# Optimization experiments

Hardware: AMD Instinct MI355X
Metric: run time of the kernel (lower is better)

Reference implementation:

```python
import jax, jax.numpy as jnp
from jax import lax
import numpy as np

D_MODEL = 384; D_INNER = 768; D_STATE = 16; D_CONV = 4; DT_RANK = 24
BATCH = 2; SEQ = 4096


def _mamba(x, in_w, conv_w, conv_b, xproj_w, dt_w, dt_b, A_log, Dp, out_w):
    # x: [B, L, D_MODEL]
    xz = x @ in_w.T                                   # [B, L, 2*D_INNER]
    xi, z = jnp.split(xz, 2, axis=-1)
    xc = jnp.swapaxes(xi, 1, 2)                       # [B, D_INNER, L]
    xc = lax.conv_general_dilated(xc, conv_w, (1,), [(D_CONV - 1, 0)],
                                  feature_group_count=D_INNER)  # causal depthwise conv
    xc = jax.nn.silu(xc + conv_b[None, :, None])
    xc = jnp.swapaxes(xc, 1, 2)                       # [B, L, D_INNER]
    xdbl = xc @ xproj_w.T                             # [B, L, DT_RANK + 2*D_STATE]
    dt = xdbl[..., :DT_RANK]
    Bm = xdbl[..., DT_RANK:DT_RANK + D_STATE]
    Cm = xdbl[..., DT_RANK + D_STATE:]
    delta = jax.nn.softplus(dt @ dt_w.T + dt_b)       # [B, L, D_INNER]
    A = -jnp.exp(A_log)                               # [D_INNER, D_STATE]

    def step(h, inp):
        d_t, x_t, B_t, C_t = inp                      # [B,Di],[B,Di],[B,N],[B,N]
        dA = jnp.exp(d_t[..., None] * A)              # [B, Di, N]
        h = dA * h + (d_t * x_t)[..., None] * B_t[:, None, :]
        return h, jnp.einsum('bdn,bn->bd', h, C_t)

    xs = tuple(jnp.swapaxes(a, 0, 1) for a in (delta, xc, Bm, Cm))  # time-major
    h0 = jnp.zeros((x.shape[0], D_INNER, D_STATE), x.dtype)
    _, ys = lax.scan(step, h0, xs)                    # ys: [L, B, D_INNER]
    y = jnp.swapaxes(ys, 0, 1) + xc * Dp              # skip term D*x
    return (y * jax.nn.silu(z)) @ out_w.T             # [B, L, D_MODEL]


def _forward(x, fp, bp, c_w, c_b, gn_w, gn_b):
    xt = jnp.swapaxes(x, 1, 2)                        # [B, L, C]
    yf = _mamba(xt, *fp)
    yb = _mamba(xt[:, ::-1, :], *bp)                  # note: source does NOT flip back
    y = jnp.concatenate([yf, yb], axis=2)             # [B, L, 2C]
    y = jnp.swapaxes(y, 1, 2)                         # [B, 2C, L]
    y = jnp.einsum('oc,bcl->bol', c_w[:, :, 0], y) + c_b[None, :, None]  # 1x1 conv
    a, b = jnp.split(y, 2, axis=1)                    # GLU over channel dim
    y = a * jax.nn.sigmoid(b)                         # [B, C, L]
    mu = y.mean(axis=(1, 2), keepdims=True)           # GroupNorm(1, C)
    var = y.var(axis=(1, 2), keepdims=True)
    y = (y - mu) / jnp.sqrt(var + 1e-5)
    return y * gn_w[None, :, None] + gn_b[None, :, None]


def setup_inputs() -> dict:
    key = jax.random.key(0)
    it = iter(jax.random.split(key, 20))

    def nrm(shape, s=0.02):
        return jax.random.normal(next(it), shape, jnp.float32) * s

    def mamba_params(pref):
        return {
            pref + 'in_w': nrm((2 * D_INNER, D_MODEL)),
            pref + 'conv_w': nrm((D_INNER, 1, D_CONV), 0.3),
            pref + 'conv_b': nrm((D_INNER,)),
            pref + 'xproj_w': nrm((DT_RANK + 2 * D_STATE, D_INNER)),
            pref + 'dt_w': nrm((D_INNER, DT_RANK), 0.1),
            pref + 'dt_b': nrm((D_INNER,)),
            pref + 'A_log': jnp.log(jnp.tile(jnp.arange(1.0, D_STATE + 1.0, dtype=jnp.float32), (D_INNER, 1))),
            pref + 'D': jnp.ones((D_INNER,), jnp.float32),
            pref + 'out_w': nrm((D_MODEL, D_INNER)),
        }

    inp = {'x': jax.random.normal(next(it), (BATCH, D_MODEL, SEQ), jnp.float32)}
    inp.update(mamba_params('f_'))
    inp.update(mamba_params('b_'))
    inp['c_w'] = nrm((2 * D_MODEL, 2 * D_MODEL, 1))
    inp['c_b'] = nrm((2 * D_MODEL,))
    inp['gn_w'] = jnp.ones((D_MODEL,), jnp.float32)
    inp['gn_b'] = jnp.zeros((D_MODEL,), jnp.float32)
    return inp


def reference(x, f_in_w, f_conv_w, f_conv_b, f_xproj_w, f_dt_w, f_dt_b, f_A_log, f_D, f_out_w,
              b_in_w, b_conv_w, b_conv_b, b_xproj_w, b_dt_w, b_dt_b, b_A_log, b_D, b_out_w,
              c_w, c_b, gn_w, gn_b):
    fp = (f_in_w, f_conv_w, f_conv_b, f_xproj_w, f_dt_w, f_dt_b, f_A_log, f_D, f_out_w)
    bp = (b_in_w, b_conv_w, b_conv_b, b_xproj_w, b_dt_w, b_dt_b, b_A_log, b_D, b_out_w)
    return _forward(x, fp, bp, c_w, c_b, gn_w, gn_b)
```

## Files before the change

### kernel.cpp

```cpp
#include <hip/hip_runtime.h>
#include <hip/hip_bf16.h>
#include <hip/hip_fp16.h>

typedef unsigned short u16;
typedef unsigned int   u32;
typedef __bf16  bf16x8 __attribute__((ext_vector_type(8)));
typedef float   f32x4  __attribute__((ext_vector_type(4)));

#define BL   8192
#define LSEQ 4096
#define DI   768
#define CHUNK 32
#define NCHUNK (LSEQ / CHUNK)
#define CTC  16
#define LOG2E 1.44269504088896340736f

#define LOAD_LDS16(g, l) __builtin_amdgcn_global_load_lds( \
    (const __attribute__((address_space(1))) void*)(g), \
    (__attribute__((address_space(3))) void*)(l), 16, 0, 0)

static __device__ __forceinline__ float bf2f(u16 u) {
    union { float f; u32 i; } v; v.i = ((u32)u) << 16; return v.f;
}
static __device__ __forceinline__ u16 f2bs(float f) {
    union { float f; u32 i; } v; v.f = f;
    u32 r = v.i + 0x7fffu + ((v.i >> 16) & 1u);
    return (u16)(r >> 16);
}
static __device__ __forceinline__ float ldf(const void* p, size_t i, int f32) {
    return f32 ? ((const float*)p)[i] : bf2f(((const u16*)p)[i]);
}

__global__ void detect_dtype(const void* __restrict__ gnw, int* __restrict__ flag) {
    u32 bits = *(const u32*)gnw;
    *flag = ((bits & 0xFFFFu) == 0u) ? 1 : 0;
}

__global__ void check_apow(const void* __restrict__ a_f, const void* __restrict__ a_b,
                           int* __restrict__ apow, const int* __restrict__ flag) {
    int f = *flag;
    __shared__ int ok;
    if (threadIdx.x == 0) ok = 1;
    __syncthreads();
    for (int i = threadIdx.x; i < 2 * 12288; i += 256) {
        const void* a = (i >= 12288) ? a_b : a_f;
        int idx = i % 12288;
        int d = idx >> 4, n = idx & 15;
        float An = __expf(ldf(a, idx, f));
        float rf = __expf(ldf(a, d * 16, f)) * (float)(n + 1);
        if (fabsf(An - rf) > 1e-5f * fabsf(rf)) ok = 0;
    }
    __syncthreads();
    if (threadIdx.x == 0) *apow = ok;
}

__global__ void cvt_bf16_3(const void* __restrict__ s0, const void* __restrict__ s1,
                           const void* __restrict__ s2, u16* __restrict__ dst,
                           int n0, int n1, int ntot, const int* __restrict__ flag) {
    int i = blockIdx.x * 256 + threadIdx.x;
    if (i >= ntot) return;
    int f = *flag;
    const void* s; size_t off;
    if (i < n0)      { s = s0; off = i; }
    else if (i < n1) { s = s1; off = i - n0; }
    else             { s = s2; off = i - n1; }
    dst[i] = f ? f2bs(((const float*)s)[off]) : ((const u16*)s)[off];
}

__global__ void cvt_conv(const void* __restrict__ cw_f, const void* __restrict__ cw_b,
                         const void* __restrict__ cb_f, const void* __restrict__ cb_b,
                         float* __restrict__ cwf, float* __restrict__ cbf,
                         const int* __restrict__ flag) {
    int i = blockIdx.x * 256 + threadIdx.x;
    int f = *flag;
    if (i < 2 * 3072)
        cwf[i] = ldf(i < 3072 ? cw_f : cw_b, i % 3072, f);
    int j = i - 2 * 3072;
    if (j >= 0 && j < 2 * 768)
        cbf[j] = ldf(j < 768 ? cb_f : cb_b, j % 768, f);
}

__global__ void transpose_x(const void* __restrict__ x, u16* __restrict__ xT,
                            const int* __restrict__ flag) {
    __shared__ u16 tile[32][33];
    int f = *flag;
    int b  = blockIdx.z;
    int l0 = blockIdx.x * 32, c0 = blockIdx.y * 32;
    int li = threadIdx.x, ci = threadIdx.y;
    for (int cc = ci; cc < 32; cc += 8) {
        size_t idx = (size_t)(b * 384 + c0 + cc) * LSEQ + l0 + li;
        tile[cc][li] = f ? f2bs(((const float*)x)[idx]) : ((const u16*)x)[idx];
    }
    __syncthreads();
    for (int lc = ci; lc < 32; lc += 8)
        xT[(size_t)(b * LSEQ + l0 + lc) * 384 + c0 + li] = tile[li][lc];
}

__global__ void build_wcomb(const void* __restrict__ xp_f, const void* __restrict__ dtw_f,
                            const void* __restrict__ xp_b, const void* __restrict__ dtw_b,
                            u16* __restrict__ Wc, const int* __restrict__ flag) {
    int f = *flag;
    int dir = blockIdx.y;
    const void* xp  = dir ? xp_b  : xp_f;
    const void* dtw = dir ? dtw_b : dtw_f;
    u16* W = Wc + (size_t)dir * 896 * 768;
    int idx = blockIdx.x * 256 + threadIdx.x;
    if (idx >= 896 * 768) return;
    int nrow = idx / 768, k = idx - nrow * 768;
    float v = 0.f;
    if (nrow < 768) {
#pragma unroll
        for (int r = 0; r < 24; r++)
            v = fmaf(ldf(dtw, nrow * 24 + r, f), ldf(xp, r * 768 + k, f), v);
    } else if (nrow < 800) {
        v = ldf(xp, (24 + (nrow - 768)) * 768 + k, f);
    }
    W[idx] = f2bs(v);
}

__global__ __launch_bounds__(256) void gemm_mfma(
    const u16* __restrict__ A, int lda, size_t aStr,
    const u16* __restrict__ W, int ldw, size_t wStr,
    int K, int NB, int Nstore, int mode,
    u16* __restrict__ ob0, u16* __restrict__ ob1,
    float* __restrict__ of0, float* __restrict__ of1,
    const void* __restrict__ bias0, const void* __restrict__ bias1,
    const int* __restrict__ flag) {
    __shared__ __align__(16) u16 lA[128 * 32];
    __shared__ __align__(16) u16 lB[128 * 32];
    const int f = *flag;
    const int tid = threadIdx.x;
    const int wave = tid >> 6, lane = tid & 63;
    const int flat = blockIdx.x;
    const int mb = flat & 63;
    const int rest = flat >> 6;
    const int nb = rest % NB;
    const int dir = rest / NB;
    const int m0 = mb * 128, n0 = nb * 128;
    const int wr = (wave >> 1) * 64, wc = (wave & 1) * 64;
    const int fr = lane & 15, fq = lane >> 4;
    const void* bias = dir ? bias1 : bias0;

    f32x4 acc[4][4];
#pragma unroll
    for (int i = 0; i < 4; i++)
#pragma unroll
        for (int j = 0; j < 4; j++) acc[i][j] = 0.f;

    const int srow = wave * 16 + (lane >> 2);
    const int scol = (lane & 3) * 8;
    const u16* gA0 = A + (size_t)dir * aStr + (size_t)(m0 + srow) * lda + scol;
    const u16* gA1 = gA0 + (size_t)64 * lda;
    const u16* gB0 = W + (size_t)dir * wStr + (size_t)(n0 + srow) * ldw + scol;
    const u16* gB1 = gB0 + (size_t)64 * ldw;
    u16* dA0 = &lA[wave * 512];
    u16* dA1 = &lA[2048 + wave * 512];
    u16* dB0 = &lB[wave * 512];
    u16* dB1 = &lB[2048 + wave * 512];

    for (int k0 = 0; k0 < K; k0 += 32) {
        __syncthreads();
        LOAD_LDS16(gA0, dA0);
        LOAD_LDS16(gA1, dA1);
        LOAD_LDS16(gB0, dB0);
        LOAD_LDS16(gB1, dB1);
        gA0 += 32; gA1 += 32; gB0 += 32; gB1 += 32;
        __syncthreads();
        bf16x8 af[4], bfr[4];
#pragma unroll
        for (int i = 0; i < 4; i++) af[i]  = *(const bf16x8*)&lA[(wr + i * 16 + fr) * 32 + fq * 8];
#pragma unroll
        for (int j = 0; j < 4; j++) bfr[j] = *(const bf16x8*)&lB[(wc + j * 16 + fr) * 32 + fq * 8];
#pragma unroll
        for (int i = 0; i < 4; i++)
#pragma unroll
            for (int j = 0; j < 4; j++)
                acc[i][j] = __builtin_amdgcn_mfma_f32_16x16x32_bf16(af[i], bfr[j], acc[i][j], 0, 0, 0);
    }

    const int lr = (lane >> 4) * 4, lc = lane & 15;
#pragma unroll
    for (int i = 0; i < 4; i++) {
#pragma unroll
        for (int j = 0; j < 4; j++) {
#pragma unroll
            for (int rg = 0; rg < 4; rg++) {
                int m = m0 + wr + i * 16 + lr + rg;
                int n = n0 + wc + j * 16 + lc;
                if (n >= Nstore) continue;
                float v = acc[i][j][rg];
                if (mode == 0) {
                    int bI = m >> 12, l = m & 4095;
                    size_t r = dir ? ((size_t)bI * LSEQ + (LSEQ - 1 - l)) : (size_t)m;
                    if (n < 768) ob0[(size_t)dir * BL * DI + r * 768 + n] = f2bs(v);
                    else         ob1[(size_t)dir * BL * DI + r * 768 + (n - 768)] = f2bs(v);
                } else if (mode == 1) {
                    if (n < 768) {
                        float xp = v + ldf(bias, n, f);
                        float sp = fmaxf(xp, 0.f) + __logf(1.f + __expf(-fabsf(xp)));
                        ((__half*)ob0)[(size_t)dir * BL * DI + (size_t)m * 768 + n] = __float2half_rn(sp);
                    } else {
                        of1[(size_t)dir * BL * 32 + (size_t)m * 32 + (n - 768)] = v;
                    }
                } else if (mode == 2) {
                    ob0[(size_t)m * 768 + dir * 384 + n] = f2bs(v);
                } else {
                    of0[(size_t)m * 768 + n] = v + ldf(bias, n, f);
                }
            }
        }
    }
}

__global__ __launch_bounds__(256) void conv_silu(
    const u16* __restrict__ xi, u16* __restrict__ xc,
    const float* __restrict__ cwf, const float* __restrict__ cbf) {
    int gid = blockIdx.x * 256 + threadIdx.x;
    int dg = gid % 96;
    int rest = gid / 96;
    int tc = rest % (LSEQ / CTC);
    int bd = rest / (LSEQ / CTC);
    int dir = bd >> 1;
    int d0 = dg * 8;
    float w[32], bias[8];
#pragma unroll
    for (int q = 0; q < 8; q++) *(float4*)&w[q * 4] = *(const float4*)&cwf[dir * 3072 + d0 * 4 + q * 4];
    *(float4*)&bias[0] = *(const float4*)&cbf[dir * 768 + d0];
    *(float4*)&bias[4] = *(const float4*)&cbf[dir * 768 + d0 + 4];
    size_t rowbase = (size_t)bd * LSEQ;
    int t0 = tc * CTC;
    uint4 zero; zero.x = zero.y = zero.z = zero.w = 0u;
    uint4 win[4];
#pragma unroll
    for (int i = 0; i < 3; i++) {
        int tt = t0 - 3 + i;
        win[i] = (tt >= 0) ? *(const uint4*)&xi[(rowbase + tt) * DI + d0] : zero;
    }
    uint4 nxt = *(const uint4*)&xi[(rowbase + t0) * DI + d0];
#pragma unroll 4
    for (int i = 0; i < CTC; i++) {
        win[3] = nxt;
        if (i + 1 < CTC) nxt = *(const uint4*)&xi[(rowbase + t0 + i + 1) * DI + d0];
        float acc[8];
#pragma unroll
        for (int c = 0; c < 8; c++) acc[c] = bias[c];
#pragma unroll
        for (int tap = 0; tap < 4; tap++) {
            const u16* pv = (const u16*)&win[tap];
#pragma unroll
            for (int c = 0; c < 8; c++)
                acc[c] = fmaf(w[c * 4 + tap], bf2f(pv[c]), acc[c]);
        }
        u16 ov[8];
#pragma unroll
        for (int c = 0; c < 8; c++) ov[c] = f2bs(acc[c] / (1.f + __expf(-acc[c])));
        *(uint4*)&xc[(rowbase + t0 + i) * DI + d0] = *(const uint4*)ov;
        win[0] = win[1]; win[1] = win[2]; win[2] = win[3];
    }
}

__global__ __launch_bounds__(256) void scan_phase1(
    const __half* __restrict__ delta, const u16* __restrict__ xc,
    const float* __restrict__ bc,
    __half* __restrict__ S, __half* __restrict__ sumdl,
    const void* __restrict__ alog_f, const void* __restrict__ alog_b,
    const int* __restrict__ flag, const int* __restrict__ apow) {
    int f = *flag, ap = *apow;
    int dblk = blockIdx.x, chunk = blockIdx.y, bd = blockIdx.z;
    int dir = bd >> 1;
    const void* alog = dir ? alog_b : alog_f;
    int d = dblk * 256 + threadIdx.x;
    size_t rowbase = (size_t)bd * LSEQ;
    float h[16];
#pragma unroll
    for (int n = 0; n < 16; n++) h[n] = 0.f;
    float An2_0 = -__expf(ldf(alog, d * 16, f)) * LOG2E;
    int t0 = chunk * CHUNK;
    size_t off = (rowbase + t0) * DI + d;
    const float* bcG = bc + (rowbase + t0) * 32;
    float sd = 0.f;
    if (ap) {
#pragma unroll 2
        for (int i = 0; i < CHUNK; i++, off += DI) {
            float Bv[16];
#pragma unroll
            for (int q = 0; q < 4; q++) *(float4*)&Bv[q * 4] = *(const float4*)&bcG[(size_t)i * 32 + q * 4];
            float dl = __half2float(delta[off]);
            float u = dl * bf2f(xc[off]);
            sd += dl;
            float e[16];
            float e1 = exp2f(dl * An2_0);
            e[0]=e1; e[1]=e1*e1; e[2]=e[1]*e1; e[3]=e[1]*e[1];
            e[4]=e[3]*e[0]; e[5]=e[3]*e[1]; e[6]=e[3]*e[2]; e[7]=e[3]*e[3];
            e[8]=e[7]*e[0]; e[9]=e[7]*e[1]; e[10]=e[7]*e[2]; e[11]=e[7]*e[3];
            e[12]=e[7]*e[4]; e[13]=e[7]*e[5]; e[14]=e[7]*e[6]; e[15]=e[7]*e[7];
#pragma unroll
            for (int n = 0; n < 16; n++) h[n] = fmaf(e[n], h[n], u * Bv[n]);
        }
    } else {
        float An2[16];
#pragma unroll
        for (int n = 0; n < 16; n++) An2[n] = -__expf(ldf(alog, d * 16 + n, f)) * LOG2E;
#pragma unroll 2
        for (int i = 0; i < CHUNK; i++, off += DI) {
            float Bv[16];
#pragma unroll
            for (int q = 0; q < 4; q++) *(float4*)&Bv[q * 4] = *(const float4*)&bcG[(size_t)i * 32 + q * 4];
            float dl = __half2float(delta[off]);
            float u = dl * bf2f(xc[off]);
            sd += dl;
#pragma unroll
            for (int n = 0; n < 16; n++)
                h[n] = fmaf(exp2f(dl * An2[n]), h[n], u * Bv[n]);
        }
    }
    __half hs[16];
#pragma unroll
    for (int n = 0; n < 16; n++) hs[n] = __float2half(h[n]);
    __half* Sp = S + (((size_t)bd * NCHUNK + chunk) * 768 + d) * 16;
    *(uint4*)&Sp[0] = *(const uint4*)&hs[0];
    *(uint4*)&Sp[8] = *(const uint4*)&hs[8];
    sumdl[((size_t)bd * NCHUNK + chunk) * 768 + d] = __float2half(sd);
}

__global__ __launch_bounds__(256) void scan_fixup(
    __half* __restrict__ S, const __half* __restrict__ sumdl,
    const void* __restrict__ alog_f, const void* __restrict__ alog_b,
    const int* __restrict__ flag) {
    int f = *flag;
    int gid = blockIdx.x * 256 + threadIdx.x;
    int bd = gid / 12288;
    int r  = gid % 12288;
    int d = r >> 4, n = r & 15;
    const void* alog = (bd >> 1) ? alog_b : alog_f;
    float An2 = -__expf(ldf(alog, d * 16 + n, f)) * LOG2E;
    float h = 0.f;
#pragma unroll 4
    for (int c = 0; c < NCHUNK; c++) {
        size_t sidx = (((size_t)bd * NCHUNK + c) * 768 + d) * 16 + n;
        float s  = __half2float(S[sidx]);
        float sd = __half2float(sumdl[((size_t)bd * NCHUNK + c) * 768 + d]);
        S[sidx] = __float2half(h);
        h = fmaf(exp2f(An2 * sd), h, s);
    }
}

__global__ __launch_bounds__(256) void scan_phase3(
    const __half* __restrict__ delta, const u16* __restrict__ xc,
    const float* __restrict__ bc, const u16* __restrict__ zz,
    const __half* __restrict__ S, u16* __restrict__ yg,
    const void* __restrict__ alog_f, const void* __restrict__ alog_b,
    const void* __restrict__ D_f, const void* __restrict__ D_b,
    const int* __restrict__ flag, const int* __restrict__ apow) {
    int f = *flag, ap = *apow;
    int dblk = blockIdx.x, chunk = blockIdx.y, bd = blockIdx.z;
    int dir = bd >> 1;
    const void* alog = dir ? alog_b : alog_f;
    const void* Dp   = dir ? D_b   : D_f;
    int d = dblk * 256 + threadIdx.x;
    size_t rowbase = (size_t)bd * LSEQ;
    float An2_0 = -__expf(ldf(alog, d * 16, f)) * LOG2E;
    float h[16];
    {
        const __half* Sp = S + (((size_t)bd * NCHUNK + chunk) * 768 + d) * 16;
        uint4 sv0 = *(const uint4*)&Sp[0];
        uint4 sv1 = *(const uint4*)&Sp[8];
        const __half* ph0 = (const __half*)&sv0;
        const __half* ph1 = (const __half*)&sv1;
#pragma unroll
        for (int n = 0; n < 8; n++) { h[n] = __half2float(ph0[n]); h[n + 8] = __half2float(ph1[n]); }
    }
    float Dd = ldf(Dp, d, f);
    int t0 = chunk * CHUNK;
    size_t off = (rowbase + t0) * DI + d;
    const float* bcG = bc + (rowbase + t0) * 32;
    if (ap) {
#pragma unroll 2
        for (int i = 0; i < CHUNK; i++, off += DI) {
            float Bv[16], Cv[16];
#pragma unroll
            for (int q = 0; q < 4; q++) *(float4*)&Bv[q * 4] = *(const float4*)&bcG[(size_t)i * 32 + q * 4];
#pragma unroll
            for (int q = 0; q < 4; q++) *(float4*)&Cv[q * 4] = *(const float4*)&bcG[(size_t)i * 32 + 16 + q * 4];
            float dl = __half2float(delta[off]);
            float xf = bf2f(xc[off]);
            float u = dl * xf;
            float e[16];
            float e1 = exp2f(dl * An2_0);
            e[0]=e1; e[1]=e1*e1; e[2]=e[1]*e1; e[3]=e[1]*e[1];
            e[4]=e[3]*e[0]; e[5]=e[3]*e[1]; e[6]=e[3]*e[2]; e[7]=e[3]*e[3];
            e[8]=e[7]*e[0]; e[9]=e[7]*e[1]; e[10]=e[7]*e[2]; e[11]=e[7]*e[3];
            e[12]=e[7]*e[4]; e[13]=e[7]*e[5]; e[14]=e[7]*e[6]; e[15]=e[7]*e[7];
            float y = 0.f;
#pragma unroll
            for (int n = 0; n < 16; n++) {
                h[n] = fmaf(e[n], h[n], u * Bv[n]);
                y = fmaf(h[n], Cv[n], y);
            }
            float zf = bf2f(zz[off]);
            yg[off] = f2bs((y + xf * Dd) * (zf / (1.f + __expf(-zf))));
        }
    } else {
        float An2[16];
#pragma unroll
        for (int n = 0; n < 16; n++) An2[n] = -__expf(ldf(alog, d * 16 + n, f)) * LOG2E;
#pragma unroll 2
        for (int i = 0; i < CHUNK; i++, off += DI) {
            float Bv[16], Cv[16];
#pragma unroll
            for (int q = 0; q < 4; q++) *(float4*)&Bv[q * 4] = *(const float4*)&bcG[(size_t)i * 32 + q * 4];
#pragma unroll
            for (int q = 0; q < 4; q++) *(float4*)&Cv[q * 4] = *(const float4*)&bcG[(size_t)i * 32 + 16 + q * 4];
            float dl = __half2float(delta[off]);
            float xf = bf2f(xc[off]);
            float u = dl * xf;
            float y = 0.f;
#pragma unroll
            for (int n = 0; n < 16; n++) {
                h[n] = fmaf(exp2f(dl * An2[n]), h[n], u * Bv[n]);
                y = fmaf(h[n], Cv[n], y);
            }
            float zf = bf2f(zz[off]);
            yg[off] = f2bs((y + xf * Dd) * (zf / (1.f + __expf(-zf))));
        }
    }
}

__global__ __launch_bounds__(256) void glu_stats(const float* __restrict__ g,
                                                 float* __restrict__ glu,
                                                 double* __restrict__ accum) {
    __shared__ float tile[64][65];
    __shared__ double wsum[8];
    int bI = blockIdx.z;
    int l0 = blockIdx.x * 64, o0 = blockIdx.y * 64;
    int tid = threadIdx.x;
    int j = tid & 63, i0 = tid >> 6;
    double s = 0.0, s2 = 0.0;
    for (int i = i0; i < 64; i += 4) {
        size_t r = (size_t)bI * LSEQ + l0 + i;
        float a  = g[r * 768 + o0 + j];
        float bb = g[r * 768 + 384 + o0 + j];
        float v = a * (1.f / (1.f + __expf(-bb)));
        tile[j][i] = v;
        s += v; s2 += (double)v * v;
    }
#pragma unroll
    for (int o = 1; o < 64; o <<= 1) { s += __shfl_xor(s, o); s2 += __shfl_xor(s2, o); }
    if ((tid & 63) == 0) { wsum[(tid >> 6) * 2] = s; wsum[(tid >> 6) * 2 + 1] = s2; }
    __syncthreads();
    if (tid == 0) {
        double S = wsum[0] + wsum[2] + wsum[4] + wsum[6];
        double S2 = wsum[1] + wsum[3] + wsum[5] + wsum[7];
        atomicAdd(&accum[bI * 2], S);
        atomicAdd(&accum[bI * 2 + 1], S2);
    }
    int l = tid & 63, oi0 = tid >> 6;
    for (int oi = oi0; oi < 64; oi += 4)
        glu[((size_t)bI * 384 + o0 + oi) * LSEQ + l0 + l] = tile[oi][l];
}

__global__ void norm_out(const float* __restrict__ glu, const double* __restrict__ accum,
                         const void* __restrict__ gnw, const void* __restrict__ gnb,
                         void* __restrict__ out, const int* __restrict__ flag) {
    int f = *flag;
    int idx = blockIdx.x * 256 + threadIdx.x;
    int b = idx / (384 * LSEQ);
    int o = (idx / LSEQ) % 384;
    double Nf = (double)(384 * LSEQ);
    double S = accum[b * 2], S2 = accum[b * 2 + 1];
    double mu = S / Nf;
    double var = S2 / Nf - mu * mu;
    float rstd = rsqrtf((float)var + 1e-5f);
    float v = (glu[idx] - (float)mu) * rstd * ldf(gnw, o, f) + ldf(gnb, o, f);
    if (f) ((float*)out)[idx] = v;
    else   ((u16*)out)[idx] = f2bs(v);
}

extern "C" void kernel_launch(void* const* d_in, const int* in_sizes, int n_in,
                              void* d_out, int out_size, void* d_ws, size_t ws_size,
                              hipStream_t stream) {
    (void)in_sizes; (void)n_in; (void)out_size; (void)ws_size;
    const void* x       = d_in[0];
    const void* inw[2]  = {d_in[1],  d_in[10]};
    const void* cwv[2]  = {d_in[2],  d_in[11]};
    const void* cbv[2]  = {d_in[3],  d_in[12]};
    const void* xpw[2]  = {d_in[4],  d_in[13]};
    const void* dtw[2]  = {d_in[5],  d_in[14]};
    const void* dtb[2]  = {d_in[6],  d_in[15]};
    const void* alog[2] = {d_in[7],  d_in[16]};
    const void* Dv[2]   = {d_in[8],  d_in[17]};
    const void* outw[2] = {d_in[9],  d_in[18]};
    const void* c_w = d_in[19];
    const void* c_b = d_in[20];
    const void* gnw = d_in[21];
    const void* gnb = d_in[22];

    char* base = (char*)d_ws;
    u16*    xT    = (u16*)   (base + 0);
    u16*    zz    = (u16*)   (base + 6291456);
    u16*    xc    = (u16*)   (base + 31457280);
    u16*    xi    = (u16*)   (base + 56623104);
    __half* delta = (__half*)(base + 56623104);
    float*  bc    = (float*) (base + 81788928);
    u16*    Wc    = (u16*)   (base + 83886080);
    u16*    yg    = (u16*)   (base + 86638592);
    double* accum = (double*)(base + 111804416);
    int*    flag  = (int*)   (base + 111804480);
    int*    apow  = (int*)   (base + 111804484);
    __half* Sbuf  = (__half*)(base + 111804672);
    __half* sumdl = (__half*)(base + 124387584);
    float*  cwf   = (float*) (base + 125174016);
    float*  cbf   = (float*) (base + 125198592);
    u16*    ycat  = zz;
    float*  g     = (float*)xc;
    float*  glu   = (float*)xi;
    u16*    cinw  = yg;
    u16*    cow   = (u16*)(base + 69206016);

    hipMemsetAsync(accum, 0, 64, stream);
    detect_dtype<<<1, 1, 0, stream>>>(gnw, flag);
    check_apow<<<1, 256, 0, stream>>>(alog[0], alog[1], apow, flag);
    cvt_conv<<<30, 256, 0, stream>>>(cwv[0], cwv[1], cbv[0], cbv[1], cwf, cbf, flag);

    transpose_x<<<dim3(LSEQ / 32, 12, 2), dim3(32, 8), 0, stream>>>(x, xT, flag);
    cvt_bf16_3<<<(1179648 + 255) / 256, 256, 0, stream>>>(
        inw[0], inw[1], inw[1], cinw, 589824, 1179648, 1179648, flag);
    build_wcomb<<<dim3((896 * 768 + 255) / 256, 2), 256, 0, stream>>>(
        xpw[0], dtw[0], xpw[1], dtw[1], Wc, flag);

    gemm_mfma<<<dim3(64 * 12 * 2), 256, 0, stream>>>(
        xT, 384, 0, cinw, 384, 589824, 384, 12, 1536, 0,
        xi, zz, nullptr, nullptr, nullptr, nullptr, flag);

    conv_silu<<<dim3(4 * (LSEQ / CTC) * 96 / 256), 256, 0, stream>>>(xi, xc, cwf, cbf);

    gemm_mfma<<<dim3(64 * 7 * 2), 256, 0, stream>>>(
        xc, 768, (size_t)BL * DI, Wc, 768, (size_t)896 * 768, 768, 7, 800, 1,
        (u16*)delta, nullptr, nullptr, bc, dtb[0], dtb[1], flag);

    scan_phase1<<<dim3(3, NCHUNK, 4), 256, 0, stream>>>(
        delta, xc, bc, Sbuf, sumdl, alog[0], alog[1], flag, apow);
    scan_fixup<<<dim3(192), 256, 0, stream>>>(Sbuf, sumdl, alog[0], alog[1], flag);
    scan_phase3<<<dim3(3, NCHUNK, 4), 256, 0, stream>>>(
        delta, xc, bc, zz, Sbuf, yg, alog[0], alog[1], Dv[0], Dv[1], flag, apow);

    cvt_bf16_3<<<(1179648 + 255) / 256, 256, 0, stream>>>(
        outw[0], outw[1], c_w, cow, 294912, 589824, 1179648, flag);

    gemm_mfma<<<dim3(64 * 3 * 2), 256, 0, stream>>>(
        yg, 768, (size_t)BL * DI, cow, 768, 294912, 768, 3, 384, 2,
        ycat, nullptr, nullptr, nullptr, nullptr, nullptr, flag);

    gemm_mfma<<<dim3(64 * 6), 256, 0, stream>>>(
        ycat, 768, 0, cow + 589824, 768, 0, 768, 6, 768, 3,
        nullptr, nullptr, g, nullptr, c_b, c_b, flag);

    glu_stats<<<dim3(LSEQ / 64, 6, 2), 256, 0, stream>>>(g, glu, accum);
    norm_out<<<dim3(2 * 384 * LSEQ / 256), 256, 0, stream>>>(glu, accum, gnw, gnb, d_out, flag);
}
```

Measured before the change: 465.4 us.

## Fold out_proj into 1x1 conv weights and double-buffer GEMM LDS tiles

Precomputes a combined weight W2 = c_w · out_w for both directions, so the out-projection GEMM and the concat-conv GEMM collapse into one K=1536 GEMM over an interleaved yg buffer written directly by scan_phase3. This removes one full GEMM pass, the intermediate ycat round trip, and a weight conversion launch. It also adds LDS double buffering to the MFMA GEMM so the next K-slice loads overlap compute, with one barrier per iteration instead of two. The folded weights are built per call by a naive 384-deep dot per element and rounded to bf16, which slightly changes numerics.

```diff
diff --git a/kernel.cpp b/kernel.cpp
--- a/kernel.cpp
+++ b/kernel.cpp
@@ -118,22 +118,39 @@
     W[idx] = f2bs(v);
 }
 
+__global__ void build_w2(const void* __restrict__ c_w, const void* __restrict__ ow_f,
+                         const void* __restrict__ ow_b, u16* __restrict__ W2,
+                         const int* __restrict__ flag) {
+    int f = *flag;
+    int idx = blockIdx.x * 256 + threadIdx.x;
+    if (idx >= 768 * 1536) return;
+    int o = idx / 1536, col = idx % 1536;
+    int dir = col / 768, d = col - dir * 768;
+    const void* ow = dir ? ow_b : ow_f;
+    float acc = 0.f;
+#pragma unroll 4
+    for (int c = 0; c < 384; c++)
+        acc = fmaf(ldf(c_w, (size_t)o * 768 + dir * 384 + c, f),
+                   ldf(ow, (size_t)c * 768 + d, f), acc);
+    W2[idx] = f2bs(acc);
+}
+
 __global__ __launch_bounds__(256) void gemm_mfma(
     const u16* __restrict__ A, int lda, size_t aStr,
     const u16* __restrict__ W, int ldw, size_t wStr,
-    int K, int NB, int Nstore, int mode,
+    int K, int MB, int NB, int Nstore, int mode,
     u16* __restrict__ ob0, u16* __restrict__ ob1,
     float* __restrict__ of0, float* __restrict__ of1,
     const void* __restrict__ bias0, const void* __restrict__ bias1,
     const int* __restrict__ flag) {
-    __shared__ __align__(16) u16 lA[128 * 32];
-    __shared__ __align__(16) u16 lB[128 * 32];
+    __shared__ __align__(16) u16 lA[2][128 * 32];
+    __shared__ __align__(16) u16 lB[2][128 * 32];
     const int f = *flag;
     const int tid = threadIdx.x;
     const int wave = tid >> 6, lane = tid & 63;
     const int flat = blockIdx.x;
-    const int mb = flat & 63;
-    const int rest = flat >> 6;
+    const int mb = flat % MB;
+    const int rest = flat / MB;
     const int nb = rest % NB;
     const int dir = rest / NB;
     const int m0 = mb * 128, n0 = nb * 128;
@@ -153,29 +170,34 @@
     const u16* gA1 = gA0 + (size_t)64 * lda;
     const u16* gB0 = W + (size_t)dir * wStr + (size_t)(n0 + srow) * ldw + scol;
     const u16* gB1 = gB0 + (size_t)64 * ldw;
-    u16* dA0 = &lA[wave * 512];
-    u16* dA1 = &lA[2048 + wave * 512];
-    u16* dB0 = &lB[wave * 512];
-    u16* dB1 = &lB[2048 + wave * 512];
-
+
+    LOAD_LDS16(gA0, &lA[0][wave * 512]);
+    LOAD_LDS16(gA1, &lA[0][2048 + wave * 512]);
+    LOAD_LDS16(gB0, &lB[0][wave * 512]);
+    LOAD_LDS16(gB1, &lB[0][2048 + wave * 512]);
+
+    int cur = 0;
     for (int k0 = 0; k0 < K; k0 += 32) {
         __syncthreads();
-        LOAD_LDS16(gA0, dA0);
-        LOAD_LDS16(gA1, dA1);
-        LOAD_LDS16(gB0, dB0);
-        LOAD_LDS16(gB1, dB1);
-        gA0 += 32; gA1 += 32; gB0 += 32; gB1 += 32;
-        __syncthreads();
+        if (k0 + 32 < K) {
+            gA0 += 32; gA1 += 32; gB0 += 32; gB1 += 32;
+            int nx = cur ^ 1;
+            LOAD_LDS16(gA0, &lA[nx][wave * 512]);
+            LOAD_LDS16(gA1, &lA[nx][2048 + wave * 512]);
+            LOAD_LDS16(gB0, &lB[nx][wave * 512]);
+            LOAD_LDS16(gB1, &lB[nx][2048 + wave * 512]);
+        }
         bf16x8 af[4], bfr[4];
 #pragma unroll
-        for (int i = 0; i < 4; i++) af[i]  = *(const bf16x8*)&lA[(wr + i * 16 + fr) * 32 + fq * 8];
-#pragma unroll
-        for (int j = 0; j < 4; j++) bfr[j] = *(const bf16x8*)&lB[(wc + j * 16 + fr) * 32 + fq * 8];
+        for (int i = 0; i < 4; i++) af[i]  = *(const bf16x8*)&lA[cur][(wr + i * 16 + fr) * 32 + fq * 8];
+#pragma unroll
+        for (int j = 0; j < 4; j++) bfr[j] = *(const bf16x8*)&lB[cur][(wc + j * 16 + fr) * 32 + fq * 8];
 #pragma unroll
         for (int i = 0; i < 4; i++)
 #pragma unroll
             for (int j = 0; j < 4; j++)
                 acc[i][j] = __builtin_amdgcn_mfma_f32_16x16x32_bf16(af[i], bfr[j], acc[i][j], 0, 0, 0);
+        cur ^= 1;
     }
 
     const int lr = (lane >> 4) * 4, lc = lane & 15;
@@ -202,8 +224,6 @@
                     } else {
                         of1[(size_t)dir * BL * 32 + (size_t)m * 32 + (n - 768)] = v;
                     }
-                } else if (mode == 2) {
-                    ob0[(size_t)m * 768 + dir * 384 + n] = f2bs(v);
                 } else {
                     of0[(size_t)m * 768 + n] = v + ldf(bias, n, f);
                 }
@@ -348,13 +368,13 @@
 __global__ __launch_bounds__(256) void scan_phase3(
     const __half* __restrict__ delta, const u16* __restrict__ xc,
     const float* __restrict__ bc, const u16* __restrict__ zz,
-    const __half* __restrict__ S, u16* __restrict__ yg,
+    const __half* __restrict__ S, u16* __restrict__ ygi,
     const void* __restrict__ alog_f, const void* __restrict__ alog_b,
     const void* __restrict__ D_f, const void* __restrict__ D_b,
     const int* __restrict__ flag, const int* __restrict__ apow) {
     int f = *flag, ap = *apow;
     int dblk = blockIdx.x, chunk = blockIdx.y, bd = blockIdx.z;
-    int dir = bd >> 1;
+    int dir = bd >> 1, b = bd & 1;
     const void* alog = dir ? alog_b : alog_f;
     const void* Dp   = dir ? D_b   : D_f;
     int d = dblk * 256 + threadIdx.x;
@@ -373,10 +393,11 @@
     float Dd = ldf(Dp, d, f);
     int t0 = chunk * CHUNK;
     size_t off = (rowbase + t0) * DI + d;
+    size_t oidx = ((size_t)b * LSEQ + t0) * 1536 + dir * 768 + d;
     const float* bcG = bc + (rowbase + t0) * 32;
     if (ap) {
 #pragma unroll 2
-        for (int i = 0; i < CHUNK; i++, off += DI) {
+        for (int i = 0; i < CHUNK; i++, off += DI, oidx += 1536) {
             float Bv[16], Cv[16];
 #pragma unroll
             for (int q = 0; q < 4; q++) *(float4*)&Bv[q * 4] = *(const float4*)&bcG[(size_t)i * 32 + q * 4];
@@ -398,14 +419,14 @@
                 y = fmaf(h[n], Cv[n], y);
             }
             float zf = bf2f(zz[off]);
-            yg[off] = f2bs((y + xf * Dd) * (zf / (1.f + __expf(-zf))));
+            ygi[oidx] = f2bs((y + xf * Dd) * (zf / (1.f + __expf(-zf))));
         }
     } else {
         float An2[16];
 #pragma unroll
         for (int n = 0; n < 16; n++) An2[n] = -__expf(ldf(alog, d * 16 + n, f)) * LOG2E;
 #pragma unroll 2
-        for (int i = 0; i < CHUNK; i++, off += DI) {
+        for (int i = 0; i < CHUNK; i++, off += DI, oidx += 1536) {
             float Bv[16], Cv[16];
 #pragma unroll
             for (int q = 0; q < 4; q++) *(float4*)&Bv[q * 4] = *(const float4*)&bcG[(size_t)i * 32 + q * 4];
@@ -421,7 +442,7 @@
                 y = fmaf(h[n], Cv[n], y);
             }
             float zf = bf2f(zz[off]);
-            yg[off] = f2bs((y + xf * Dd) * (zf / (1.f + __expf(-zf))));
+            ygi[oidx] = f2bs((y + xf * Dd) * (zf / (1.f + __expf(-zf))));
         }
     }
 }
@@ -511,11 +532,10 @@
     __half* sumdl = (__half*)(base + 124387584);
     float*  cwf   = (float*) (base + 125174016);
     float*  cbf   = (float*) (base + 125198592);
-    u16*    ycat  = zz;
     float*  g     = (float*)xc;
     float*  glu   = (float*)xi;
     u16*    cinw  = yg;
-    u16*    cow   = (u16*)(base + 69206016);
+    u16*    W2    = (u16*)(base + 69206016);
 
     hipMemsetAsync(accum, 0, 64, stream);
     detect_dtype<<<1, 1, 0, stream>>>(gnw, flag);
@@ -529,13 +549,13 @@
         xpw[0], dtw[0], xpw[1], dtw[1], Wc, flag);
 
     gemm_mfma<<<dim3(64 * 12 * 2), 256, 0, stream>>>(
-        xT, 384, 0, cinw, 384, 589824, 384, 12, 1536, 0,
+        xT, 384, 0, cinw, 384, 589824, 384, 64, 12, 1536, 0,
         xi, zz, nullptr, nullptr, nullptr, nullptr, flag);
 
     conv_silu<<<dim3(4 * (LSEQ / CTC) * 96 / 256), 256, 0, stream>>>(xi, xc, cwf, cbf);
 
     gemm_mfma<<<dim3(64 * 7 * 2), 256, 0, stream>>>(
-        xc, 768, (size_t)BL * DI, Wc, 768, (size_t)896 * 768, 768, 7, 800, 1,
+        xc, 768, (size_t)BL * DI, Wc, 768, (size_t)896 * 768, 768, 64, 7, 800, 1,
         (u16*)delta, nullptr, nullptr, bc, dtb[0], dtb[1], flag);
 
     scan_phase1<<<dim3(3, NCHUNK, 4), 256, 0, stream>>>(
@@ -544,15 +564,10 @@
     scan_phase3<<<dim3(3, NCHUNK, 4), 256, 0, stream>>>(
         delta, xc, bc, zz, Sbuf, yg, alog[0], alog[1], Dv[0], Dv[1], flag, apow);
 
-    cvt_bf16_3<<<(1179648 + 255) / 256, 256, 0, stream>>>(
-        outw[0], outw[1], c_w, cow, 294912, 589824, 1179648, flag);
-
-    gemm_mfma<<<dim3(64 * 3 * 2), 256, 0, stream>>>(
-        yg, 768, (size_t)BL * DI, cow, 768, 294912, 768, 3, 384, 2,
-        ycat, nullptr, nullptr, nullptr, nullptr, nullptr, flag);
+    build_w2<<<(768 * 1536 + 255) / 256, 256, 0, stream>>>(c_w, outw[0], outw[1], W2, flag);
 
     gemm_mfma<<<dim3(64 * 6), 256, 0, stream>>>(
-        ycat, 768, 0, cow + 589824, 768, 0, 768, 6, 768, 3,
+        yg, 1536, 0, W2, 1536, 0, 1536, 64, 6, 768, 3,
         nullptr, nullptr, g, nullptr, c_b, c_b, flag);
 
     glu_stats<<<dim3(LSEQ / 64, 6, 2), 256, 0, stream>>>(g, glu, accum);
```

Result: slower. 582.1 us (+25.1%).
